# Kernel optimization log

Hardware: AMD Instinct MI355X
Metric: run time of the kernel (lower is better)

Reference implementation:

```python
import jax, jax.numpy as jnp
import numpy as np

H = 768   # hidden_size
B, E, M = 4, 42, 16   # batch, entity_limit, mention_limit
S_LIM = 25
N = 4096  # flattened head-tail pairs
NEG = -1e9


def setup_inputs() -> dict:
    key = jax.random.key(0)
    ks = jax.random.split(key, 12)
    inp = {
        "entity_embed": jax.random.normal(ks[0], (B, E, H), jnp.float32),
        "mention_embed": jax.random.normal(ks[1], (B, E, M, H), jnp.float32),
        "sent_embed": jax.random.normal(ks[2], (B, S_LIM, H), jnp.float32),
        "entity_info": jax.random.randint(ks[3], (B, E, 7), 0, 25, jnp.int64) if jax.config.jax_enable_x64 else jax.random.randint(ks[3], (B, E, 7), 0, 25).astype(jnp.int32),
        "mention_num": jax.random.randint(ks[4], (B, E), 1, M + 1),  # >=1 mention per entity
        "b_ind": jax.random.randint(ks[5], (N,), 0, B),
        "h_ind": jax.random.randint(ks[6], (N,), 0, E),
        "t_ind": jax.random.randint(ks[7], (N,), 0, E),
        # parameters (torch Linear: y = x @ W.T), bias=False everywhere
        "W_head": jax.random.normal(ks[8], (H, H), jnp.float32) / np.sqrt(H),
        "W_tail": jax.random.normal(ks[9], (H, H), jnp.float32) / np.sqrt(H),
        "w_c": jax.random.normal(ks[10], (H,), jnp.float32) / np.sqrt(H),
        "w_q": jax.random.normal(ks[11], (H,), jnp.float32) / np.sqrt(H),
        "w_cq": jax.random.normal(jax.random.fold_in(key, 99), (H,), jnp.float32) / np.sqrt(H),
    }
    return inp


def reference(entity_embed, mention_embed, sent_embed, entity_info,
              mention_num, b_ind, h_ind, t_ind,
              W_head, W_tail, w_c, w_q, w_cq):
    m_lim = mention_embed.shape[-2]
    hfo = mention_embed[b_ind, h_ind]          # [N, M, H]
    tfo = mention_embed[b_ind, t_ind]          # [N, M, H]
    hf = jax.nn.relu(jnp.einsum('nmh,oh->nmo', hfo, W_head))
    tf = jax.nn.relu(jnp.einsum('nmh,oh->nmo', tfo, W_tail))

    # Original loop: cq[n,m,i] = w_cq . (hf[n,m,i] * tf[n,m,:]) = hf[n,m,i] * (tf[n,m,:].w_cq)
    # (faithful to the source's select(2, i) over the hidden dim)
    tq = tf @ w_cq                              # [N, M]
    cq = tq[:, :, None] * hf[:, :, :m_lim]      # [N, M, M]

    s = (hf @ w_c)[:, :, None] + (tf @ w_q)[:, None, :] + cq  # [N, M, M]

    idx = jnp.arange(m_lim)
    head_num = mention_num[b_ind, h_ind]        # [N]
    tail_num = mention_num[b_ind, t_ind]        # [N]
    s = jnp.where(idx[None, :, None] >= head_num[:, None, None], NEG, s)
    s = jnp.where(idx[None, None, :] >= tail_num[:, None, None], NEG, s)

    h_weight = jax.nn.softmax(jnp.max(s, axis=-1), axis=-1)   # [N, M]
    start_re_output = jnp.einsum('nm,nmh->nh', h_weight, hf)  # [N, H]
    t_weight = jax.nn.softmax(jnp.max(s, axis=-2), axis=-1)   # [N, M]
    end_re_output = jnp.einsum('nm,nmh->nh', t_weight, tf)    # [N, H]

    head_embed = jnp.concatenate([entity_embed[b_ind, h_ind], start_re_output], axis=-1)
    tail_embed = jnp.concatenate([entity_embed[b_ind, t_ind], end_re_output], axis=-1)
    return head_embed, tail_embed
```

## Files before the change

kernel.cpp:

```cpp
#include <hip/hip_runtime.h>
#include <hip/hip_bf16.h>

#define Hd   768
#define Bsz  4
#define Ent  42
#define Mm   16
#define NEGV (-1e9f)

#define GM 2688
#define GN 1536
#define GK 768
#define NT (GK / 32)

typedef short bf16x8 __attribute__((ext_vector_type(8)));
typedef float f32x4  __attribute__((ext_vector_type(4)));
typedef unsigned short u16x8 __attribute__((ext_vector_type(8)));
typedef unsigned short u16x4 __attribute__((ext_vector_type(4)));

static __device__ __forceinline__ unsigned short f2bf(float x) {
    unsigned int u = __float_as_uint(x);
    u += 0x7fffu + ((u >> 16) & 1u);
    return (unsigned short)(u >> 16);
}
static __device__ __forceinline__ float bf2f(unsigned short v) {
    return __uint_as_float(((unsigned int)v) << 16);
}

__global__ __launch_bounds__(256)
void to_bf16(const float* __restrict__ me, const float* __restrict__ wh,
             const float* __restrict__ wt, unsigned short* __restrict__ dst)
{
    const int t = blockIdx.x * 256 + threadIdx.x;
    const size_t e = (size_t)t * 8;
    const size_t row = e / Hd;
    const float* src;
    size_t off;
    if (row < 2688)      { src = me; off = e; }
    else if (row < 3456) { src = wh; off = e - (size_t)2688 * Hd; }
    else                 { src = wt; off = e - (size_t)3456 * Hd; }
    float4 v0 = *reinterpret_cast<const float4*>(src + off);
    float4 v1 = *reinterpret_cast<const float4*>(src + off + 4);
    u16x8 o;
    o[0] = f2bf(v0.x); o[1] = f2bf(v0.y); o[2] = f2bf(v0.z); o[3] = f2bf(v0.w);
    o[4] = f2bf(v1.x); o[5] = f2bf(v1.y); o[6] = f2bf(v1.z); o[7] = f2bf(v1.w);
    *reinterpret_cast<u16x8*>(dst + e) = o;
}

__global__ __launch_bounds__(256)
void gemm_mfma(const unsigned short* __restrict__ Ab,
               const unsigned short* __restrict__ Wb,
               unsigned short* __restrict__ f_head,
               unsigned short* __restrict__ f_tail)
{
    __shared__ unsigned short As[2][64 * 32];
    __shared__ unsigned short Bs[2][128 * 32];

    const int tid  = threadIdx.x;
    const int wave = tid >> 6;
    const int lane = tid & 63;
    const int n0 = blockIdx.x * 128;
    const int m0 = blockIdx.y * 64;

    const int srow = wave * 16 + (lane >> 2);
    const int scol = (lane & 3) * 8;
    const unsigned short* Aga = Ab + (size_t)(m0 + srow) * GK + scol;
    const unsigned short* Bga = Wb + (size_t)(n0 + srow) * GK + scol;

#define STAGE(buf, k0) do { \
    __builtin_amdgcn_global_load_lds((const __attribute__((address_space(1))) void*)(Aga + (k0)), \
        (__attribute__((address_space(3))) void*)(As[buf] + wave * 512), 16, 0, 0); \
    __builtin_amdgcn_global_load_lds((const __attribute__((address_space(1))) void*)(Bga + (k0)), \
        (__attribute__((address_space(3))) void*)(Bs[buf] + wave * 512), 16, 0, 0); \
    __builtin_amdgcn_global_load_lds((const __attribute__((address_space(1))) void*)(Bga + 64 * GK + (k0)), \
        (__attribute__((address_space(3))) void*)(Bs[buf] + 2048 + wave * 512), 16, 0, 0); \
} while (0)

    const int frow = lane & 15;
    const int koff = (lane >> 4) * 8;

    f32x4 acc[4][2];
    {
        f32x4 z = {0.f, 0.f, 0.f, 0.f};
        #pragma unroll
        for (int mi = 0; mi < 4; ++mi) { acc[mi][0] = z; acc[mi][1] = z; }
    }

    STAGE(0, 0);
    int cur = 0;
    #pragma unroll 1
    for (int t = 0; t < NT; ++t) {
        __syncthreads();
        if (t < NT - 1) STAGE(cur ^ 1, (t + 1) * 32);
        const unsigned short* ap = As[cur] + frow * 32 + koff;
        const unsigned short* bp = Bs[cur] + (wave * 32 + frow) * 32 + koff;
        bf16x8 a[4], b[2];
        #pragma unroll
        for (int mi = 0; mi < 4; ++mi)
            a[mi] = *reinterpret_cast<const bf16x8*>(ap + mi * 16 * 32);
        b[0] = *reinterpret_cast<const bf16x8*>(bp);
        b[1] = *reinterpret_cast<const bf16x8*>(bp + 16 * 32);
        #pragma unroll
        for (int mi = 0; mi < 4; ++mi) {
            acc[mi][0] = __builtin_amdgcn_mfma_f32_16x16x32_bf16(a[mi], b[0], acc[mi][0], 0, 0, 0);
            acc[mi][1] = __builtin_amdgcn_mfma_f32_16x16x32_bf16(a[mi], b[1], acc[mi][1], 0, 0, 0);
        }
        cur ^= 1;
    }
#undef STAGE

    const bool isHead = (n0 < Hd);
    unsigned short* outp = isHead ? f_head : f_tail;
    const int nbase = (isHead ? n0 : (n0 - Hd)) + wave * 32 + frow;
    const int rbase = m0 + (lane >> 4) * 4;
    #pragma unroll
    for (int mi = 0; mi < 4; ++mi)
        #pragma unroll
        for (int ni = 0; ni < 2; ++ni)
            #pragma unroll
            for (int j = 0; j < 4; ++j) {
                float v = fmaxf(acc[mi][ni][j], 0.f);
                outp[(size_t)(rbase + mi * 16 + j) * Hd + nbase + ni * 16] = f2bf(v);
            }
}

__global__ __launch_bounds__(256)
void row_dots(const unsigned short* __restrict__ f_head,
              const unsigned short* __restrict__ f_tail,
              const float* __restrict__ w_c, const float* __restrict__ w_q,
              const float* __restrict__ w_cq,
              float* __restrict__ ch, float* __restrict__ qt, float* __restrict__ cqt)
{
    const int wave = threadIdx.x >> 6;
    const int lane = threadIdx.x & 63;
    const int r = blockIdx.x * 4 + wave;
    const unsigned short* fh = f_head + (size_t)r * Hd;
    const unsigned short* ft = f_tail + (size_t)r * Hd;
    float pc = 0.f, pq = 0.f, pcq = 0.f;
    #pragma unroll
    for (int j = 0; j < Hd / 64; ++j) {
        const int c = j * 64 + lane;
        float vh = bf2f(fh[c]), vt = bf2f(ft[c]);
        pc += vh * w_c[c]; pq += vt * w_q[c]; pcq += vt * w_cq[c];
    }
    #pragma unroll
    for (int s = 32; s >= 1; s >>= 1) {
        pc  += __shfl_down(pc, s);
        pq  += __shfl_down(pq, s);
        pcq += __shfl_down(pcq, s);
    }
    if (lane == 0) { ch[r] = pc; qt[r] = pq; cqt[r] = pcq; }
}

__global__ __launch_bounds__(256)
void pair_attn(const unsigned short* __restrict__ f_head,
               const unsigned short* __restrict__ f_tail,
               const float* __restrict__ ch, const float* __restrict__ qt,
               const float* __restrict__ cqt,
               const float* __restrict__ entity_embed,
               const int* __restrict__ mention_num,
               const int* __restrict__ b_ind, const int* __restrict__ h_ind,
               const int* __restrict__ t_ind,
               float* __restrict__ out, int N)
{
    const int tid  = threadIdx.x;
    const int wave = tid >> 6;
    const int lane = tid & 63;

    __shared__ float hwS[4][16];
    __shared__ float twS[4][16];

    int n = blockIdx.x * 4 + wave;
    if (n >= N) n = N - 1;

    const int b = b_ind[n], h = h_ind[n], t = t_ind[n];
    const int eh = b * Ent + h, et = b * Ent + t;
    const int rh = eh * Mm, rt = et * Mm;
    const int hn = mention_num[eh], tn = mention_num[et];

    const int i  = lane >> 2;
    const int jg = lane & 3;

    const float chi = ch[rh + i];
    const float cqi = cqt[rt + i];
    const float4 q4 = *reinterpret_cast<const float4*>(qt + rt + jg * 4);
    const u16x4 f4  = *reinterpret_cast<const u16x4*>(
                          f_head + (size_t)(rh + i) * Hd + jg * 4);
    float v[4];
    #pragma unroll
    for (int k = 0; k < 4; ++k) {
        const int j = jg * 4 + k;
        const float qv = (k == 0) ? q4.x : (k == 1) ? q4.y : (k == 2) ? q4.z : q4.w;
        v[k] = (i < hn && j < tn) ? (chi + qv + cqi * bf2f(f4[k])) : NEGV;
    }

    float rm = fmaxf(fmaxf(v[0], v[1]), fmaxf(v[2], v[3]));
    rm = fmaxf(rm, __shfl_xor(rm, 1));
    rm = fmaxf(rm, __shfl_xor(rm, 2));

    float cm[4];
    #pragma unroll
    for (int k = 0; k < 4; ++k) {
        cm[k] = v[k];
        cm[k] = fmaxf(cm[k], __shfl_xor(cm[k], 4));
        cm[k] = fmaxf(cm[k], __shfl_xor(cm[k], 8));
        cm[k] = fmaxf(cm[k], __shfl_xor(cm[k], 16));
        cm[k] = fmaxf(cm[k], __shfl_xor(cm[k], 32));
    }

    float gm = rm;
    gm = fmaxf(gm, __shfl_xor(gm, 4));
    gm = fmaxf(gm, __shfl_xor(gm, 8));
    gm = fmaxf(gm, __shfl_xor(gm, 16));
    gm = fmaxf(gm, __shfl_xor(gm, 32));
    const float eh_ = expf(rm - gm);
    float S = eh_;
    S += __shfl_xor(S, 4);
    S += __shfl_xor(S, 8);
    S += __shfl_xor(S, 16);
    S += __shfl_xor(S, 32);
    const float hwv = eh_ / S;

    float gmt = fmaxf(fmaxf(cm[0], cm[1]), fmaxf(cm[2], cm[3]));
    gmt = fmaxf(gmt, __shfl_xor(gmt, 1));
    gmt = fmaxf(gmt, __shfl_xor(gmt, 2));
    float et_[4];
    float St = 0.f;
    #pragma unroll
    for (int k = 0; k < 4; ++k) { et_[k] = expf(cm[k] - gmt); St += et_[k]; }
    St += __shfl_xor(St, 1);
    St += __shfl_xor(St, 2);

    if (jg == 0) hwS[wave][i] = hwv;
    if (lane < 4) {
        #pragma unroll
        for (int k = 0; k < 4; ++k) twS[wave][lane * 4 + k] = et_[k] / St;
    }
    __syncthreads();

    const size_t oh = (size_t)n * (2 * Hd);
    const size_t ot = (size_t)(N + n) * (2 * Hd);
    const unsigned short* fhp = f_head + (size_t)rh * Hd;
    const unsigned short* ftp = f_tail + (size_t)rt * Hd;

    #pragma unroll
    for (int c = 0; c < 3; ++c) {
        const int col = c * 256 + lane * 4;
        float a0 = 0.f, a1 = 0.f, a2 = 0.f, a3 = 0.f;
        for (int ii = 0; ii < hn; ++ii) {
            const u16x4 fv = *reinterpret_cast<const u16x4*>(fhp + (size_t)ii * Hd + col);
            const float w = hwS[wave][ii];
            a0 += w * bf2f(fv[0]); a1 += w * bf2f(fv[1]);
            a2 += w * bf2f(fv[2]); a3 += w * bf2f(fv[3]);
        }
        float4 o = {a0, a1, a2, a3};
        *reinterpret_cast<float4*>(out + oh + Hd + col) = o;
    }
    #pragma unroll
    for (int c = 0; c < 3; ++c) {
        const int col = c * 256 + lane * 4;
        float a0 = 0.f, a1 = 0.f, a2 = 0.f, a3 = 0.f;
        for (int ii = 0; ii < tn; ++ii) {
            const u16x4 fv = *reinterpret_cast<const u16x4*>(ftp + (size_t)ii * Hd + col);
            const float w = twS[wave][ii];
            a0 += w * bf2f(fv[0]); a1 += w * bf2f(fv[1]);
            a2 += w * bf2f(fv[2]); a3 += w * bf2f(fv[3]);
        }
        float4 o = {a0, a1, a2, a3};
        *reinterpret_cast<float4*>(out + ot + Hd + col) = o;
    }

    const float4* ehp = reinterpret_cast<const float4*>(entity_embed + (size_t)eh * Hd);
    const float4* etp = reinterpret_cast<const float4*>(entity_embed + (size_t)et * Hd);
    #pragma unroll
    for (int c = 0; c < 3; ++c) {
        const int g = c * 64 + lane;
        reinterpret_cast<float4*>(out + oh)[g] = ehp[g];
        reinterpret_cast<float4*>(out + ot)[g] = etp[g];
    }
}

extern "C" void kernel_launch(void* const* d_in, const int* in_sizes, int n_in,
                              void* d_out, int out_size, void* d_ws, size_t ws_size,
                              hipStream_t stream)
{
    const float* entity_embed  = (const float*)d_in[0];
    const float* mention_embed = (const float*)d_in[1];
    const int*   mention_num   = (const int*)d_in[4];
    const int*   b_ind         = (const int*)d_in[5];
    const int*   h_ind         = (const int*)d_in[6];
    const int*   t_ind         = (const int*)d_in[7];
    const float* W_head        = (const float*)d_in[8];
    const float* W_tail        = (const float*)d_in[9];
    const float* w_c           = (const float*)d_in[10];
    const float* w_q           = (const float*)d_in[11];
    const float* w_cq          = (const float*)d_in[12];
    float* out = (float*)d_out;

    const int N = in_sizes[5];

    unsigned short* Ab     = (unsigned short*)d_ws;
    unsigned short* Wb     = Ab + (size_t)GM * GK;
    unsigned short* f_head = Wb + (size_t)GN * GK;
    unsigned short* f_tail = f_head + (size_t)GM * Hd;
    float* ch  = (float*)(f_tail + (size_t)GM * Hd);
    float* qt  = ch + GM;
    float* cqt = qt + GM;

    to_bf16<<<(GM + GN) * GK / (8 * 256), 256, 0, stream>>>(
        mention_embed, W_head, W_tail, Ab);

    dim3 gg(GN / 128, GM / 64);
    gemm_mfma<<<gg, 256, 0, stream>>>(Ab, Wb, f_head, f_tail);

    row_dots<<<GM / 4, 256, 0, stream>>>(f_head, f_tail, w_c, w_q, w_cq, ch, qt, cqt);

    pair_attn<<<(N + 3) / 4, 256, 0, stream>>>(f_head, f_tail, ch, qt, cqt,
                                               entity_embed, mention_num,
                                               b_ind, h_ind, t_ind, out, N);
}
```

Before: 50.65 us.

## Fuse row-dot reductions into GEMM epilogue and load MFMA operands directly

Removes the separate row_dots kernel by computing the w_c, w_q and w_cq dot products in the GEMM epilogue from fp32 accumulators. Partial sums are reduced with shuffles and combined across blocks with atomicAdd into buffers that the conversion kernel now zeroes. The GEMM also drops LDS double buffering and loads bf16x8 fragments straight from global memory in a fully unrolled K loop. This saves a launch and a re-read of the features, at the cost of atomics, nondeterministic summation order and less cache-friendly operand loads.

```diff
diff --git a/kernel.cpp b/kernel.cpp
--- a/kernel.cpp
+++ b/kernel.cpp
@@ -28,9 +28,14 @@
 
 __global__ __launch_bounds__(256)
 void to_bf16(const float* __restrict__ me, const float* __restrict__ wh,
-             const float* __restrict__ wt, unsigned short* __restrict__ dst)
+             const float* __restrict__ wt, unsigned short* __restrict__ dst,
+             float* __restrict__ dots)
 {
     const int t = blockIdx.x * 256 + threadIdx.x;
+    if (t < 3 * GM / 4) {
+        float4 z = {0.f, 0.f, 0.f, 0.f};
+        reinterpret_cast<float4*>(dots)[t] = z;
+    }
     const size_t e = (size_t)t * 8;
     const size_t row = e / Hd;
     const float* src;
@@ -47,36 +52,31 @@
 }
 
 __global__ __launch_bounds__(256)
-void gemm_mfma(const unsigned short* __restrict__ Ab,
-               const unsigned short* __restrict__ Wb,
-               unsigned short* __restrict__ f_head,
-               unsigned short* __restrict__ f_tail)
+void gemm_direct(const unsigned short* __restrict__ Ab,
+                 const unsigned short* __restrict__ Wb,
+                 unsigned short* __restrict__ f_head,
+                 unsigned short* __restrict__ f_tail,
+                 const float* __restrict__ w_c, const float* __restrict__ w_q,
+                 const float* __restrict__ w_cq,
+                 float* __restrict__ ch, float* __restrict__ qt,
+                 float* __restrict__ cqt)
 {
-    __shared__ unsigned short As[2][64 * 32];
-    __shared__ unsigned short Bs[2][128 * 32];
-
     const int tid  = threadIdx.x;
     const int wave = tid >> 6;
     const int lane = tid & 63;
     const int n0 = blockIdx.x * 128;
     const int m0 = blockIdx.y * 64;
-
-    const int srow = wave * 16 + (lane >> 2);
-    const int scol = (lane & 3) * 8;
-    const unsigned short* Aga = Ab + (size_t)(m0 + srow) * GK + scol;
-    const unsigned short* Bga = Wb + (size_t)(n0 + srow) * GK + scol;
-
-#define STAGE(buf, k0) do { \
-    __builtin_amdgcn_global_load_lds((const __attribute__((address_space(1))) void*)(Aga + (k0)), \
-        (__attribute__((address_space(3))) void*)(As[buf] + wave * 512), 16, 0, 0); \
-    __builtin_amdgcn_global_load_lds((const __attribute__((address_space(1))) void*)(Bga + (k0)), \
-        (__attribute__((address_space(3))) void*)(Bs[buf] + wave * 512), 16, 0, 0); \
-    __builtin_amdgcn_global_load_lds((const __attribute__((address_space(1))) void*)(Bga + 64 * GK + (k0)), \
-        (__attribute__((address_space(3))) void*)(Bs[buf] + 2048 + wave * 512), 16, 0, 0); \
-} while (0)
-
     const int frow = lane & 15;
-    const int koff = (lane >> 4) * 8;
+    const int kg   = lane >> 4;
+    const int koff = kg * 8;
+
+    const unsigned short* ar0 = Ab + (size_t)(m0 +  0 + frow) * GK + koff;
+    const unsigned short* ar1 = Ab + (size_t)(m0 + 16 + frow) * GK + koff;
+    const unsigned short* ar2 = Ab + (size_t)(m0 + 32 + frow) * GK + koff;
+    const unsigned short* ar3 = Ab + (size_t)(m0 + 48 + frow) * GK + koff;
+    const int nb = n0 + wave * 32 + frow;
+    const unsigned short* br0 = Wb + (size_t)nb * GK + koff;
+    const unsigned short* br1 = Wb + (size_t)(nb + 16) * GK + koff;
 
     f32x4 acc[4][2];
     {
@@ -85,70 +85,70 @@
         for (int mi = 0; mi < 4; ++mi) { acc[mi][0] = z; acc[mi][1] = z; }
     }
 
-    STAGE(0, 0);
-    int cur = 0;
-    #pragma unroll 1
+    #pragma unroll
     for (int t = 0; t < NT; ++t) {
-        __syncthreads();
-        if (t < NT - 1) STAGE(cur ^ 1, (t + 1) * 32);
-        const unsigned short* ap = As[cur] + frow * 32 + koff;
-        const unsigned short* bp = Bs[cur] + (wave * 32 + frow) * 32 + koff;
-        bf16x8 a[4], b[2];
-        #pragma unroll
-        for (int mi = 0; mi < 4; ++mi)
-            a[mi] = *reinterpret_cast<const bf16x8*>(ap + mi * 16 * 32);
-        b[0] = *reinterpret_cast<const bf16x8*>(bp);
-        b[1] = *reinterpret_cast<const bf16x8*>(bp + 16 * 32);
-        #pragma unroll
-        for (int mi = 0; mi < 4; ++mi) {
-            acc[mi][0] = __builtin_amdgcn_mfma_f32_16x16x32_bf16(a[mi], b[0], acc[mi][0], 0, 0, 0);
-            acc[mi][1] = __builtin_amdgcn_mfma_f32_16x16x32_bf16(a[mi], b[1], acc[mi][1], 0, 0, 0);
-        }
-        cur ^= 1;
-    }
-#undef STAGE
+        const int kb = t * 32;
+        bf16x8 a0 = *reinterpret_cast<const bf16x8*>(ar0 + kb);
+        bf16x8 a1 = *reinterpret_cast<const bf16x8*>(ar1 + kb);
+        bf16x8 a2 = *reinterpret_cast<const bf16x8*>(ar2 + kb);
+        bf16x8 a3 = *reinterpret_cast<const bf16x8*>(ar3 + kb);
+        bf16x8 b0 = *reinterpret_cast<const bf16x8*>(br0 + kb);
+        bf16x8 b1 = *reinterpret_cast<const bf16x8*>(br1 + kb);
+        acc[0][0] = __builtin_amdgcn_mfma_f32_16x16x32_bf16(a0, b0, acc[0][0], 0, 0, 0);
+        acc[0][1] = __builtin_amdgcn_mfma_f32_16x16x32_bf16(a0, b1, acc[0][1], 0, 0, 0);
+        acc[1][0] = __builtin_amdgcn_mfma_f32_16x16x32_bf16(a1, b0, acc[1][0], 0, 0, 0);
+        acc[1][1] = __builtin_amdgcn_mfma_f32_16x16x32_bf16(a1, b1, acc[1][1], 0, 0, 0);
+        acc[2][0] = __builtin_amdgcn_mfma_f32_16x16x32_bf16(a2, b0, acc[2][0], 0, 0, 0);
+        acc[2][1] = __builtin_amdgcn_mfma_f32_16x16x32_bf16(a2, b1, acc[2][1], 0, 0, 0);
+        acc[3][0] = __builtin_amdgcn_mfma_f32_16x16x32_bf16(a3, b0, acc[3][0], 0, 0, 0);
+        acc[3][1] = __builtin_amdgcn_mfma_f32_16x16x32_bf16(a3, b1, acc[3][1], 0, 0, 0);
+    }
 
     const bool isHead = (n0 < Hd);
     unsigned short* outp = isHead ? f_head : f_tail;
-    const int nbase = (isHead ? n0 : (n0 - Hd)) + wave * 32 + frow;
-    const int rbase = m0 + (lane >> 4) * 4;
+    const int nloc = (isHead ? n0 : (n0 - Hd)) + wave * 32 + frow;
+    const int rbase = m0 + kg * 4;
+
+    const float* w0 = isHead ? w_c : w_q;
+    const float w0a = w0[nloc], w0b = w0[nloc + 16];
+    const float w1a = isHead ? 0.f : w_cq[nloc];
+    const float w1b = isHead ? 0.f : w_cq[nloc + 16];
+
+    float p0[4][4], p1[4][4];
     #pragma unroll
     for (int mi = 0; mi < 4; ++mi)
         #pragma unroll
-        for (int ni = 0; ni < 2; ++ni)
+        for (int j = 0; j < 4; ++j) {
+            const float va = fmaxf(acc[mi][0][j], 0.f);
+            const float vb = fmaxf(acc[mi][1][j], 0.f);
+            const size_t r = (size_t)(rbase + mi * 16 + j) * Hd + nloc;
+            outp[r]      = f2bf(va);
+            outp[r + 16] = f2bf(vb);
+            p0[mi][j] = va * w0a + vb * w0b;
+            p1[mi][j] = va * w1a + vb * w1b;
+        }
+
+    #pragma unroll
+    for (int s = 1; s <= 8; s <<= 1)
+        #pragma unroll
+        for (int mi = 0; mi < 4; ++mi)
             #pragma unroll
             for (int j = 0; j < 4; ++j) {
-                float v = fmaxf(acc[mi][ni][j], 0.f);
-                outp[(size_t)(rbase + mi * 16 + j) * Hd + nbase + ni * 16] = f2bf(v);
+                p0[mi][j] += __shfl_xor(p0[mi][j], s);
+                if (!isHead) p1[mi][j] += __shfl_xor(p1[mi][j], s);
             }
-}
-
-__global__ __launch_bounds__(256)
-void row_dots(const unsigned short* __restrict__ f_head,
-              const unsigned short* __restrict__ f_tail,
-              const float* __restrict__ w_c, const float* __restrict__ w_q,
-              const float* __restrict__ w_cq,
-              float* __restrict__ ch, float* __restrict__ qt, float* __restrict__ cqt)
-{
-    const int wave = threadIdx.x >> 6;
-    const int lane = threadIdx.x & 63;
-    const int r = blockIdx.x * 4 + wave;
-    const unsigned short* fh = f_head + (size_t)r * Hd;
-    const unsigned short* ft = f_tail + (size_t)r * Hd;
-    float pc = 0.f, pq = 0.f, pcq = 0.f;
-    #pragma unroll
-    for (int j = 0; j < Hd / 64; ++j) {
-        const int c = j * 64 + lane;
-        float vh = bf2f(fh[c]), vt = bf2f(ft[c]);
-        pc += vh * w_c[c]; pq += vt * w_q[c]; pcq += vt * w_cq[c];
-    }
-    #pragma unroll
-    for (int s = 32; s >= 1; s >>= 1) {
-        pc  += __shfl_down(pc, s);
-        pq  += __shfl_down(pq, s);
-        pcq += __shfl_down(pcq, s);
-    }
-    if (lane == 0) { ch[r] = pc; qt[r] = pq; cqt[r] = pcq; }
+
+    if (frow == 0) {
+        float* d0 = isHead ? ch : qt;
+        #pragma unroll
+        for (int mi = 0; mi < 4; ++mi)
+            #pragma unroll
+            for (int j = 0; j < 4; ++j) {
+                const int r = rbase + mi * 16 + j;
+                atomicAdd(&d0[r], p0[mi][j]);
+                if (!isHead) atomicAdd(&cqt[r], p1[mi][j]);
+            }
+    }
 }
 
 __global__ __launch_bounds__(256)
@@ -307,12 +307,11 @@
     float* cqt = qt + GM;
 
     to_bf16<<<(GM + GN) * GK / (8 * 256), 256, 0, stream>>>(
-        mention_embed, W_head, W_tail, Ab);
+        mention_embed, W_head, W_tail, Ab, ch);
 
     dim3 gg(GN / 128, GM / 64);
-    gemm_mfma<<<gg, 256, 0, stream>>>(Ab, Wb, f_head, f_tail);
-
-    row_dots<<<GM / 4, 256, 0, stream>>>(f_head, f_tail, w_c, w_q, w_cq, ch, qt, cqt);
+    gemm_direct<<<gg, 256, 0, stream>>>(Ab, Wb, f_head, f_tail,
+                                        w_c, w_q, w_cq, ch, qt, cqt);
 
     pair_attn<<<(N + 3) / 4, 256, 0, stream>>>(f_head, f_tail, ch, qt, cqt,
                                                entity_embed, mention_num,
```

Measured after the change: 70.86 us. +39.9%, slower.

## Double GEMM K-tile to 64 and XOR-swizzle LDS layout

Applied to the files above, without the earlier changes.

The bf16 MFMA GEMM now stages 64-wide K tiles instead of 32, which halves the number of barrier-separated iterations. It also stores each row in LDS with an XOR swizzle on the 16-byte chunk index to avoid bank conflicts on the fragment reads. Each wave issues six global-to-LDS loads per stage and runs twice as many MFMAs between barriers. In exchange, LDS use per block doubles, which may reduce occupancy.

```diff
diff --git a/kernel.cpp b/kernel.cpp
--- a/kernel.cpp
+++ b/kernel.cpp
@@ -10,7 +10,7 @@
 #define GM 2688
 #define GN 1536
 #define GK 768
-#define NT (GK / 32)
+#define NT2 (GK / 64)
 
 typedef short bf16x8 __attribute__((ext_vector_type(8)));
 typedef float f32x4  __attribute__((ext_vector_type(4)));
@@ -52,8 +52,8 @@
                unsigned short* __restrict__ f_head,
                unsigned short* __restrict__ f_tail)
 {
-    __shared__ unsigned short As[2][64 * 32];
-    __shared__ unsigned short Bs[2][128 * 32];
+    __shared__ unsigned short As[2][64 * 64];
+    __shared__ unsigned short Bs[2][128 * 64];
 
     const int tid  = threadIdx.x;
     const int wave = tid >> 6;
@@ -61,22 +61,31 @@
     const int n0 = blockIdx.x * 128;
     const int m0 = blockIdx.y * 64;
 
-    const int srow = wave * 16 + (lane >> 2);
-    const int scol = (lane & 3) * 8;
-    const unsigned short* Aga = Ab + (size_t)(m0 + srow) * GK + scol;
-    const unsigned short* Bga = Wb + (size_t)(n0 + srow) * GK + scol;
+    const int sr8   = lane >> 3;
+    const int scolE = ((lane & 7) ^ sr8) * 8;
+    const unsigned short* AgaBase = Ab + (size_t)(m0 + wave * 16 + sr8) * GK + scolE;
+    const unsigned short* BgaBase = Wb + (size_t)(n0 + wave * 32 + sr8) * GK + scolE;
 
 #define STAGE(buf, k0) do { \
-    __builtin_amdgcn_global_load_lds((const __attribute__((address_space(1))) void*)(Aga + (k0)), \
-        (__attribute__((address_space(3))) void*)(As[buf] + wave * 512), 16, 0, 0); \
-    __builtin_amdgcn_global_load_lds((const __attribute__((address_space(1))) void*)(Bga + (k0)), \
-        (__attribute__((address_space(3))) void*)(Bs[buf] + wave * 512), 16, 0, 0); \
-    __builtin_amdgcn_global_load_lds((const __attribute__((address_space(1))) void*)(Bga + 64 * GK + (k0)), \
-        (__attribute__((address_space(3))) void*)(Bs[buf] + 2048 + wave * 512), 16, 0, 0); \
+    __builtin_amdgcn_global_load_lds((const __attribute__((address_space(1))) void*)(AgaBase + (k0)), \
+        (__attribute__((address_space(3))) void*)(As[buf] + (wave * 16) * 64), 16, 0, 0); \
+    __builtin_amdgcn_global_load_lds((const __attribute__((address_space(1))) void*)(AgaBase + 8 * GK + (k0)), \
+        (__attribute__((address_space(3))) void*)(As[buf] + (wave * 16 + 8) * 64), 16, 0, 0); \
+    __builtin_amdgcn_global_load_lds((const __attribute__((address_space(1))) void*)(BgaBase + (k0)), \
+        (__attribute__((address_space(3))) void*)(Bs[buf] + (wave * 32) * 64), 16, 0, 0); \
+    __builtin_amdgcn_global_load_lds((const __attribute__((address_space(1))) void*)(BgaBase + 8 * GK + (k0)), \
+        (__attribute__((address_space(3))) void*)(Bs[buf] + (wave * 32 + 8) * 64), 16, 0, 0); \
+    __builtin_amdgcn_global_load_lds((const __attribute__((address_space(1))) void*)(BgaBase + 16 * GK + (k0)), \
+        (__attribute__((address_space(3))) void*)(Bs[buf] + (wave * 32 + 16) * 64), 16, 0, 0); \
+    __builtin_amdgcn_global_load_lds((const __attribute__((address_space(1))) void*)(BgaBase + 24 * GK + (k0)), \
+        (__attribute__((address_space(3))) void*)(Bs[buf] + (wave * 32 + 24) * 64), 16, 0, 0); \
 } while (0)
 
     const int frow = lane & 15;
-    const int koff = (lane >> 4) * 8;
+    const int kg   = lane >> 4;
+    const int f7x  = (frow & 7) << 4;
+    const int rdE0 = ((kg * 16)      ^ f7x) >> 1;
+    const int rdE1 = ((kg * 16 + 64) ^ f7x) >> 1;
 
     f32x4 acc[4][2];
     {
@@ -88,22 +97,29 @@
     STAGE(0, 0);
     int cur = 0;
     #pragma unroll 1
-    for (int t = 0; t < NT; ++t) {
+    for (int t = 0; t < NT2; ++t) {
         __syncthreads();
-        if (t < NT - 1) STAGE(cur ^ 1, (t + 1) * 32);
-        const unsigned short* ap = As[cur] + frow * 32 + koff;
-        const unsigned short* bp = Bs[cur] + (wave * 32 + frow) * 32 + koff;
-        bf16x8 a[4], b[2];
-        #pragma unroll
-        for (int mi = 0; mi < 4; ++mi)
-            a[mi] = *reinterpret_cast<const bf16x8*>(ap + mi * 16 * 32);
-        b[0] = *reinterpret_cast<const bf16x8*>(bp);
-        b[1] = *reinterpret_cast<const bf16x8*>(bp + 16 * 32);
+        if (t < NT2 - 1) STAGE(cur ^ 1, (t + 1) * 64);
+        const unsigned short* a_ = As[cur] + frow * 64;
+        const unsigned short* b_ = Bs[cur] + (wave * 32 + frow) * 64;
+        bf16x8 a[4][2], b[2][2];
         #pragma unroll
         for (int mi = 0; mi < 4; ++mi) {
-            acc[mi][0] = __builtin_amdgcn_mfma_f32_16x16x32_bf16(a[mi], b[0], acc[mi][0], 0, 0, 0);
-            acc[mi][1] = __builtin_amdgcn_mfma_f32_16x16x32_bf16(a[mi], b[1], acc[mi][1], 0, 0, 0);
+            a[mi][0] = *reinterpret_cast<const bf16x8*>(a_ + mi * 16 * 64 + rdE0);
+            a[mi][1] = *reinterpret_cast<const bf16x8*>(a_ + mi * 16 * 64 + rdE1);
         }
+        #pragma unroll
+        for (int ni = 0; ni < 2; ++ni) {
+            b[ni][0] = *reinterpret_cast<const bf16x8*>(b_ + ni * 16 * 64 + rdE0);
+            b[ni][1] = *reinterpret_cast<const bf16x8*>(b_ + ni * 16 * 64 + rdE1);
+        }
+        #pragma unroll
+        for (int kk = 0; kk < 2; ++kk)
+            #pragma unroll
+            for (int mi = 0; mi < 4; ++mi) {
+                acc[mi][0] = __builtin_amdgcn_mfma_f32_16x16x32_bf16(a[mi][kk], b[0][kk], acc[mi][0], 0, 0, 0);
+                acc[mi][1] = __builtin_amdgcn_mfma_f32_16x16x32_bf16(a[mi][kk], b[1][kk], acc[mi][1], 0, 0, 0);
+            }
         cur ^= 1;
     }
 #undef STAGE
@@ -111,7 +127,7 @@
     const bool isHead = (n0 < Hd);
     unsigned short* outp = isHead ? f_head : f_tail;
     const int nbase = (isHead ? n0 : (n0 - Hd)) + wave * 32 + frow;
-    const int rbase = m0 + (lane >> 4) * 4;
+    const int rbase = m0 + kg * 4;
     #pragma unroll
     for (int mi = 0; mi < 4; ++mi)
         #pragma unroll
```

After: 47.04 us. 7.1% less time.
